# Performance work log

Measured on AMD Instinct MI355X. Metric: run time of the kernel, lower is better.

Reference implementation:

```python
import jax, jax.numpy as jnp
import numpy as np

S = 30.0   # scale
M = 0.3    # additive angular margin (arcface)
EPS = 1e-07


def setup_inputs() -> dict:
    key = jax.random.key(0)
    k1, k2, k3 = jax.random.split(key, 3)
    N, D, C = 8192, 256, 10000
    x = jax.random.normal(k1, (N, D), dtype=jnp.float32)
    W = jax.random.normal(k2, (C, D), dtype=jnp.float32) * 0.05  # linear weight [C, D]
    target = jax.random.randint(k3, (N,), 0, C)
    return {"x": x, "W": W, "target": target}


def reference(x, W, target):
    # L2-normalize inputs along features. NOTE: the torch code's loop that
    # 'normalizes' weight_fc params is a no-op (rebinds a local), so W is
    # intentionally NOT normalized here, matching the original math.
    xn = x / jnp.linalg.norm(x, axis=1, keepdims=True)
    logits = xn @ W.T                                   # [N, C]
    n = logits.shape[0]
    tgt = logits[jnp.arange(n), target]                 # [N] target-class cosine-like score
    # arcface margin: s * cos(acos(clamp(t)) + m)
    numerator = S * jnp.cos(jnp.arccos(jnp.clip(tgt, -1.0 + EPS, 1.0 - EPS)) + M)
    # exclude-target sum: sum_j exp(s*logits) minus the target column (no [N,C-1] concat)
    exp_s = jnp.exp(S * logits)                         # [N, C]
    sum_excl = jnp.sum(exp_s, axis=1) - jnp.exp(S * tgt)
    denominator = jnp.exp(numerator) + sum_excl
    L = numerator - jnp.log(denominator)
    return -jnp.mean(L)
```

## Files before the change

kernel.cpp:

```cpp
#include <hip/hip_runtime.h>
#include <hip/hip_bf16.h>
#include <stdint.h>

#define S_SCALE 30.0f
#define XSC 360.0f
#define WSC 400.0f
#define SC_EPI 3.00561467e-4f
#define N_ROWS 8192
#define D_DIM 256
#define C_CLS 10000
#define NCB 8

typedef __attribute__((ext_vector_type(4))) int i32x4;

static __device__ __forceinline__ void gl16(const void* g, void* l) {
  __builtin_amdgcn_global_load_lds(
      (const __attribute__((address_space(1))) void*)g,
      (__attribute__((address_space(3))) void*)l, 16, 0, 0);
}

static __device__ __forceinline__ int q4(float a, float b, float c, float d) {
  int qa = (int)rintf(fminf(fmaxf(a, -127.f), 127.f));
  int qb = (int)rintf(fminf(fmaxf(b, -127.f), 127.f));
  int qc = (int)rintf(fminf(fmaxf(c, -127.f), 127.f));
  int qd = (int)rintf(fminf(fmaxf(d, -127.f), 127.f));
  return (qa & 255) | ((qb & 255) << 8) | ((qc & 255) << 16) | ((qd & 255) << 24);
}

static __device__ __forceinline__ float row_sum16(float v) {
  union { float f; int i; } u, w;
  u.f = v;
  w.i = __builtin_amdgcn_update_dpp(0, u.i, 0xB1, 0xF, 0xF, true);  u.f += w.f;
  w.i = __builtin_amdgcn_update_dpp(0, u.i, 0x4E, 0xF, 0xF, true);  u.f += w.f;
  w.i = __builtin_amdgcn_update_dpp(0, u.i, 0x141, 0xF, 0xF, true); u.f += w.f;
  w.i = __builtin_amdgcn_update_dpp(0, u.i, 0x140, 0xF, 0xF, true); u.f += w.f;
  return u.f;
}

__global__ __launch_bounds__(256) void k_prep(const float* __restrict__ x,
                                              const float* __restrict__ W,
                                              const int* __restrict__ target,
                                              unsigned char* __restrict__ xnb8,
                                              unsigned char* __restrict__ WbF8,
                                              float* __restrict__ tgt) {
  if (blockIdx.x < 1280) {
    int gidx = blockIdx.x * 256 + threadIdx.x;
    int sub = gidx & 1;
    int lane = (gidx >> 1) & 63;
    int kchunk = (gidx >> 7) & 3;
    int c16 = gidx >> 9;
    int col = c16 * 16 + (lane & 15);
    int k0 = kchunk * 64 + (lane >> 4) * 16 + sub * 8;
    int r0 = 0, r1 = 0;
    if (col < C_CLS) {
      const float4 a = *(const float4*)(W + (size_t)col * D_DIM + k0);
      const float4 b = *(const float4*)(W + (size_t)col * D_DIM + k0 + 4);
      r0 = q4(a.x * WSC, a.y * WSC, a.z * WSC, a.w * WSC);
      r1 = q4(b.x * WSC, b.y * WSC, b.z * WSC, b.w * WSC);
    }
    size_t dst = (size_t)c16 * 4096 + (size_t)kchunk * 1024 +
                 (size_t)lane * 16 + (size_t)sub * 8;
    *(int2*)(WbF8 + dst) = (int2){r0, r1};
  } else {
    int row = (blockIdx.x - 1280) * 4 + (threadIdx.x >> 6);
    int l = threadIdx.x & 63;
    const float4 v = *(const float4*)(x + (size_t)row * D_DIM + l * 4);
    float ss = v.x * v.x + v.y * v.y + v.z * v.z + v.w * v.w;
#pragma unroll
    for (int m = 1; m < 64; m <<= 1) ss += __shfl_xor(ss, m, 64);
    float rn = 1.0f / sqrtf(ss);
    float s8 = rn * XSC;
    int r0 = q4(v.x * s8, v.y * s8, v.z * s8, v.w * s8);
    int panel = row >> 7, r16 = (row >> 4) & 7, lr = row & 15;
    int kchunk = l >> 4;
    int lk = (l >> 2) & 3;
    int byte = (l & 3) * 4;
    size_t dst = (size_t)panel * 32768 + (size_t)(r16 * 4 + kchunk) * 1024 +
                 (size_t)(lk * 16 + lr) * 16 + byte;
    *(int*)(xnb8 + dst) = r0;
    int tc = target[row];
    const float4 b = *(const float4*)(W + (size_t)tc * D_DIM + l * 4);
    float s = v.x * b.x + v.y * b.y + v.z * b.z + v.w * b.w;
#pragma unroll
    for (int m = 1; m < 64; m <<= 1) s += __shfl_xor(s, m, 64);
    if (l == 0) tgt[row] = s * rn;
  }
}

__global__ __launch_bounds__(512, 4) void k_gemm(const unsigned char* __restrict__ xnb8,
                                                 const unsigned char* __restrict__ WbF8,
                                                 float* __restrict__ partials) {
  __shared__ __align__(16) char lds[34816];
  const int b = blockIdx.x;
  const int cg = b & 7;
  const int br = b >> 3;
  const int bc0 = cg * 5;
  const int t = threadIdx.x;
  const int w = t >> 6, l = t & 63;
  const int wr = w >> 2, wc = w & 3;
  const int lr = l & 15, lk = l >> 4;
  float* rsumAll = (float*)(lds + 32768);

  if (t < 512) rsumAll[t] = 0.f;

  {
    const char* Ag = (const char*)xnb8 + (size_t)br * 32768;
#pragma unroll
    for (int i = 0; i < 4; ++i)
      gl16(Ag + i * 8192 + w * 1024 + l * 16, lds + i * 8192 + w * 1024);
    asm volatile("s_waitcnt vmcnt(0)" ::: "memory");
    __builtin_amdgcn_sched_barrier(0);
    __builtin_amdgcn_s_barrier();
  }

  i32x4 acc[4][4];
  const i32x4 zi = (i32x4){0, 0, 0, 0};

  const char* AwL = lds + (size_t)wr * 16384 + (size_t)l * 16;
  const unsigned char* Bw = WbF8 + (size_t)(bc0 * 16 + wc * 4) * 4096 + (size_t)l * 16;
  float* rw = rsumAll + w * 64;

  for (int tt = 0; tt < 5; ++tt) {
    const unsigned char* Bt = Bw + (size_t)tt * 65536;

    auto windw = [&](int kc, bool first) {
      i32x4 bf[4];
#pragma unroll
      for (int fn = 0; fn < 4; ++fn)
        bf[fn] = *(const i32x4*)(Bt + fn * 4096 + kc * 1024);
      __builtin_amdgcn_s_setprio(1);
#pragma unroll
      for (int fm = 0; fm < 4; ++fm) {
        i32x4 a = *(const i32x4*)(AwL + (fm * 4 + kc) * 1024);
#pragma unroll
        for (int fn = 0; fn < 4; ++fn)
          acc[fm][fn] = __builtin_amdgcn_mfma_i32_16x16x64_i8(
              a, bf[fn], first ? zi : acc[fm][fn], 0, 0, 0);
      }
      __builtin_amdgcn_s_setprio(0);
    };
    windw(0, true); windw(1, false); windw(2, false); windw(3, false);

#pragma unroll
    for (int m = 0; m < 4; ++m) {
      float rs0 = 0.f, rs1 = 0.f, rs2 = 0.f, rs3 = 0.f;
#pragma unroll
      for (int n = 0; n < 4; ++n) {
        rs0 += __builtin_amdgcn_exp2f((float)acc[m][n][0] * SC_EPI);
        rs1 += __builtin_amdgcn_exp2f((float)acc[m][n][1] * SC_EPI);
        rs2 += __builtin_amdgcn_exp2f((float)acc[m][n][2] * SC_EPI);
        rs3 += __builtin_amdgcn_exp2f((float)acc[m][n][3] * SC_EPI);
      }
      rs0 = row_sum16(rs0); rs1 = row_sum16(rs1);
      rs2 = row_sum16(rs2); rs3 = row_sum16(rs3);
      if (lr == 0) {
        int row = m * 16 + lk * 4;
        rw[row + 0] += rs0; rw[row + 1] += rs1;
        rw[row + 2] += rs2; rw[row + 3] += rs3;
      }
    }
  }

  __syncthreads();
  if (t < 128) {
    int wr2 = t >> 6, r = t & 63;
    float sv = rsumAll[(wr2 * 4 + 0) * 64 + r] + rsumAll[(wr2 * 4 + 1) * 64 + r] +
               rsumAll[(wr2 * 4 + 2) * 64 + r] + rsumAll[(wr2 * 4 + 3) * 64 + r];
    partials[(size_t)cg * N_ROWS + (size_t)br * 128 + t] = sv;
  }
}

__global__ __launch_bounds__(256) void k_loss1(const float* __restrict__ partials,
                                               const float* __restrict__ tgt,
                                               float* __restrict__ bsum) {
  __shared__ float wsum[4];
  int i = blockIdx.x * 256 + threadIdx.x;
  const float* p = partials + i;
  float s = -240.0f;
#pragma unroll
  for (int j = 0; j < NCB; ++j) s += p[(size_t)j * N_ROWS];
  float tl = tgt[i];
  float tcv = fminf(fmaxf(tl, -1.0f + 1e-7f), 1.0f - 1e-7f);
  const float cm = 0.95533648912560601964f;
  const float sm = 0.29552020666133957510f;
  float num = S_SCALE * (tcv * cm - sqrtf(fmaxf(1.0f - tcv * tcv, 0.f)) * sm);
  float sum_excl = s - __expf(S_SCALE * tl);
  float denom = __expf(num) + sum_excl;
  float L = num - __logf(denom);
#pragma unroll
  for (int m = 1; m < 64; m <<= 1) L += __shfl_xor(L, m, 64);
  int l = threadIdx.x & 63, w = threadIdx.x >> 6;
  if (l == 0) wsum[w] = L;
  __syncthreads();
  if (threadIdx.x == 0) bsum[blockIdx.x] = wsum[0] + wsum[1] + wsum[2] + wsum[3];
}

__global__ void k_loss2(const float* __restrict__ bsum, float* __restrict__ out) {
  float s = 0.f;
  for (int i = 0; i < 32; ++i) s += bsum[i];
  out[0] = -s / (float)N_ROWS;
}

extern "C" void kernel_launch(void* const* d_in, const int* in_sizes, int n_in,
                              void* d_out, int out_size, void* d_ws, size_t ws_size,
                              hipStream_t stream) {
  const float* x = (const float*)d_in[0];
  const float* W = (const float*)d_in[1];
  const int* target = (const int*)d_in[2];
  float* out = (float*)d_out;
  char* ws = (char*)d_ws;

  unsigned char* xnb8 = (unsigned char*)(ws);
  unsigned char* WbF8 = (unsigned char*)(ws + 2097152);
  float* tgt = (float*)(ws + 4718592);
  float* partials = (float*)(ws + 4751360);
  float* bsum = (float*)(ws + 5013504);

  k_prep<<<3328, 256, 0, stream>>>(x, W, target, xnb8, WbF8, tgt);
  k_gemm<<<512, 512, 0, stream>>>(xnb8, WbF8, partials);
  k_loss1<<<32, 256, 0, stream>>>(partials, tgt, bsum);
  k_loss2<<<1, 1, 0, stream>>>(bsum, out);
}
```

Measured before the change: 44.10 us.

## Split GEMM blocks to 256 threads and software-prefetch B fragments

The GEMM kernel now uses 256-thread blocks (4 waves in a 2x2 layout), twice as many blocks, and splits each column group into two halves, so there are 16 partial column blocks instead of 8. B fragments are double-buffered in registers and the next k-chunk, or the next tile, is loaded ahead of the MFMAs that consume the current one, so global-load latency can hide behind compute. The changes are meant to improve latency hiding and how the blocks spread across CUs. In exchange there is more register pressure, each block loads the A panel separately so A is reloaded more often, and the loss kernel has twice as many partial sums to combine.

```diff
diff --git a/kernel.cpp b/kernel.cpp
--- a/kernel.cpp
+++ b/kernel.cpp
@@ -9,7 +9,7 @@
 #define N_ROWS 8192
 #define D_DIM 256
 #define C_CLS 10000
-#define NCB 8
+#define NCB 16
 
 typedef __attribute__((ext_vector_type(4))) int i32x4;
 
@@ -87,27 +87,27 @@
   }
 }
 
-__global__ __launch_bounds__(512, 4) void k_gemm(const unsigned char* __restrict__ xnb8,
+__global__ __launch_bounds__(256, 3) void k_gemm(const unsigned char* __restrict__ xnb8,
                                                  const unsigned char* __restrict__ WbF8,
                                                  float* __restrict__ partials) {
-  __shared__ __align__(16) char lds[34816];
+  __shared__ __align__(16) char lds[33792];
   const int b = blockIdx.x;
   const int cg = b & 7;
-  const int br = b >> 3;
-  const int bc0 = cg * 5;
+  const int sub = (b >> 3) & 1;
+  const int br = b >> 4;
   const int t = threadIdx.x;
   const int w = t >> 6, l = t & 63;
-  const int wr = w >> 2, wc = w & 3;
+  const int wr = w >> 1, wc = w & 1;
   const int lr = l & 15, lk = l >> 4;
   float* rsumAll = (float*)(lds + 32768);
 
-  if (t < 512) rsumAll[t] = 0.f;
+  rsumAll[t] = 0.f;
 
   {
     const char* Ag = (const char*)xnb8 + (size_t)br * 32768;
 #pragma unroll
-    for (int i = 0; i < 4; ++i)
-      gl16(Ag + i * 8192 + w * 1024 + l * 16, lds + i * 8192 + w * 1024);
+    for (int i = 0; i < 8; ++i)
+      gl16(Ag + i * 4096 + w * 1024 + l * 16, lds + i * 4096 + w * 1024);
     asm volatile("s_waitcnt vmcnt(0)" ::: "memory");
     __builtin_amdgcn_sched_barrier(0);
     __builtin_amdgcn_s_barrier();
@@ -117,17 +117,28 @@
   const i32x4 zi = (i32x4){0, 0, 0, 0};
 
   const char* AwL = lds + (size_t)wr * 16384 + (size_t)l * 16;
-  const unsigned char* Bw = WbF8 + (size_t)(bc0 * 16 + wc * 4) * 4096 + (size_t)l * 16;
+  const unsigned char* Bw = WbF8 + (size_t)((cg * 2 + sub) * 40 + wc * 4) * 4096 +
+                            (size_t)l * 16;
   float* rw = rsumAll + w * 64;
 
+  i32x4 P[4], Q[4], R[4], S[4];
+#pragma unroll
+  for (int fn = 0; fn < 4; ++fn) {
+    P[fn] = *(const i32x4*)(Bw + fn * 4096);
+    Q[fn] = *(const i32x4*)(Bw + fn * 4096 + 1024);
+  }
+
   for (int tt = 0; tt < 5; ++tt) {
-    const unsigned char* Bt = Bw + (size_t)tt * 65536;
-
-    auto windw = [&](int kc, bool first) {
-      i32x4 bf[4];
-#pragma unroll
-      for (int fn = 0; fn < 4; ++fn)
-        bf[fn] = *(const i32x4*)(Bt + fn * 4096 + kc * 1024);
+    const unsigned char* Bt = Bw + (size_t)tt * 32768;
+    const bool nx = (tt < 4);
+
+    auto windw = [&](int kc, bool first, i32x4(&cur)[4], i32x4(&pre)[4],
+                     int preOff, bool doPre) {
+      if (doPre) {
+#pragma unroll
+        for (int fn = 0; fn < 4; ++fn)
+          pre[fn] = *(const i32x4*)(Bt + fn * 4096 + preOff);
+      }
       __builtin_amdgcn_s_setprio(1);
 #pragma unroll
       for (int fm = 0; fm < 4; ++fm) {
@@ -135,11 +146,14 @@
 #pragma unroll
         for (int fn = 0; fn < 4; ++fn)
           acc[fm][fn] = __builtin_amdgcn_mfma_i32_16x16x64_i8(
-              a, bf[fn], first ? zi : acc[fm][fn], 0, 0, 0);
+              a, cur[fn], first ? zi : acc[fm][fn], 0, 0, 0);
       }
       __builtin_amdgcn_s_setprio(0);
     };
-    windw(0, true); windw(1, false); windw(2, false); windw(3, false);
+    windw(0, true,  P, R, 2 * 1024, true);
+    windw(1, false, Q, S, 3 * 1024, true);
+    windw(2, false, R, P, 32768 + 0, nx);
+    windw(3, false, S, Q, 32768 + 1024, nx);
 
 #pragma unroll
     for (int m = 0; m < 4; ++m) {
@@ -164,9 +178,8 @@
   __syncthreads();
   if (t < 128) {
     int wr2 = t >> 6, r = t & 63;
-    float sv = rsumAll[(wr2 * 4 + 0) * 64 + r] + rsumAll[(wr2 * 4 + 1) * 64 + r] +
-               rsumAll[(wr2 * 4 + 2) * 64 + r] + rsumAll[(wr2 * 4 + 3) * 64 + r];
-    partials[(size_t)cg * N_ROWS + (size_t)br * 128 + t] = sv;
+    float sv = rsumAll[(wr2 * 2 + 0) * 64 + r] + rsumAll[(wr2 * 2 + 1) * 64 + r];
+    partials[(size_t)(cg * 2 + sub) * N_ROWS + (size_t)br * 128 + t] = sv;
   }
 }
 
@@ -214,10 +227,10 @@
   unsigned char* WbF8 = (unsigned char*)(ws + 2097152);
   float* tgt = (float*)(ws + 4718592);
   float* partials = (float*)(ws + 4751360);
-  float* bsum = (float*)(ws + 5013504);
+  float* bsum = (float*)(ws + 5275648);
 
   k_prep<<<3328, 256, 0, stream>>>(x, W, target, xnb8, WbF8, tgt);
-  k_gemm<<<512, 512, 0, stream>>>(xnb8, WbF8, partials);
+  k_gemm<<<1024, 256, 0, stream>>>(xnb8, WbF8, partials);
   k_loss1<<<32, 256, 0, stream>>>(partials, tgt, bsum);
   k_loss2<<<1, 1, 0, stream>>>(bsum, out);
 }
```

New measurement: 45.77 us. +3.8%, slower.
